# Kernel optimization log

Measured on AMD Instinct MI355X. Metric: run time of the kernel, lower is better.

Reference implementation:

```python
import jax, jax.numpy as jnp
import numpy as np

HW = 1048576   # h*w pixels (1024x1024)
C = 64         # feature channels
K = 4096       # number of superpixel clusters (min_superpixels)
H1 = 256       # KAN hidden width
NCLS = 16      # output classes
G = 5          # grid_size
SO = 3         # spline_order


def _grid(in_features):
    # torch: (arange(-SO, G+SO+1) * h + grid_range[0]).expand(in_features, -1)
    h = 2.0 / G  # (grid_range[1]-grid_range[0])/grid_size
    g = jnp.arange(-SO, G + SO + 1, dtype=jnp.float32) * h - 1.0  # [G+2*SO+1]
    return jnp.broadcast_to(g, (in_features, G + 2 * SO + 1))


def _b_splines(x, grid):
    # x: [N, in] -> bases: [N, in, G+SO]
    xg = x[:, :, None]
    bases = ((xg >= grid[:, :-1]) & (xg < grid[:, 1:])).astype(x.dtype)
    for k in range(1, SO + 1):
        left = (xg - grid[:, :-(k + 1)]) / (grid[:, k:-1] - grid[:, :-(k + 1)])
        right = (grid[:, k + 1:] - xg) / (grid[:, k + 1:] - grid[:, 1:-k])
        bases = left * bases[:, :, :-1] + right * bases[:, :, 1:]
    return bases


def _kan_layer(x, base_w, spline_w, spline_scaler):
    # KANLinear.forward: silu(x) @ base_w.T + bsplines(x) . (spline_w * scaler)
    grid = _grid(x.shape[-1])
    base_out = jax.nn.silu(x) @ base_w.T                      # [N, out]
    bases = _b_splines(x, grid)                               # [N, in, G+SO]
    scaled_w = spline_w * spline_scaler[:, :, None]           # [out, in, G+SO]
    spline_out = jnp.einsum('nig,oig->no', bases, scaled_w)
    return base_out + spline_out


def setup_inputs() -> dict:
    key = jax.random.key(0)
    ks = jax.random.split(key, 8)
    x = jax.random.normal(ks[0], (HW, C), dtype=jnp.float32)
    cls = jax.random.randint(ks[1], (HW,), 0, K, dtype=jnp.int32)
    bw1 = jax.random.normal(ks[2], (H1, C), dtype=jnp.float32) * 0.1
    sw1 = jax.random.normal(ks[3], (H1, C, G + SO), dtype=jnp.float32) * 0.1
    sc1 = jax.random.normal(ks[4], (H1, C), dtype=jnp.float32) * 0.1
    bw2 = jax.random.normal(ks[5], (NCLS, H1), dtype=jnp.float32) * 0.1
    sw2 = jax.random.normal(ks[6], (NCLS, H1, G + SO), dtype=jnp.float32) * 0.1
    sc2 = jax.random.normal(ks[7], (NCLS, H1), dtype=jnp.float32) * 0.1
    return dict(x=x, cls=cls, bw1=bw1, sw1=sw1, sc1=sc1, bw2=bw2, sw2=sw2, sc2=sc2)


def reference(x, cls, bw1, sw1, sc1, bw2, sw2, sc2):
    # VDSM scatter-mean aggregation: per-cluster mean of pixel features
    sums = jax.ops.segment_sum(x, cls, num_segments=K)                       # [K, C]
    cnt = jax.ops.segment_sum(jnp.ones((HW,), x.dtype), cls, num_segments=K)  # [K]
    clus_feat = sums / jnp.maximum(cnt, 1.0)[:, None]
    # WIC_Cls: stack of KANLinear layers on cluster features
    h = _kan_layer(clus_feat, bw1, sw1, sc1)
    out = _kan_layer(h, bw2, sw2, sc2)
    return out
```

## Files before the change

kernel.cpp:

```cpp
#include <hip/hip_runtime.h>

#define HW_N 1048576
#define C_IN 64
#define K_CLS 4096
#define H1_N 256
#define NCLS_N 16
#define SCAT_BLOCKS 256
#define ROWS_PER_SCAT (HW_N / SCAT_BLOCKS)
#define CAP 512
#define CLPB 16

__device__ __forceinline__ float silu_f(float x) {
  return x / (1.0f + expf(-x));
}

__device__ __forceinline__ void bspline8(float x, float* b) {
  float t[11];
#pragma unroll
  for (int j = 0; j < 11; ++j) {
    float g0 = 0.4f * (float)(j - 3) - 1.0f;
    float g1 = 0.4f * (float)(j - 2) - 1.0f;
    t[j] = (x >= g0 && x < g1) ? 1.0f : 0.0f;
  }
#pragma unroll
  for (int k = 1; k <= 3; ++k) {
#pragma unroll 10
    for (int j = 0; j + k < 11; ++j) {
      float gj   = 0.4f * (float)(j - 3) - 1.0f;
      float gj1  = 0.4f * (float)(j - 2) - 1.0f;
      float gjk  = 0.4f * (float)(j + k - 3) - 1.0f;
      float gjk1 = 0.4f * (float)(j + k - 2) - 1.0f;
      float left  = (x - gj) / (gjk - gj);
      float right = (gjk1 - x) / (gjk1 - gj1);
      t[j] = left * t[j] + right * t[j + 1];
    }
  }
#pragma unroll
  for (int g = 0; g < 8; ++g) b[g] = t[g];
}

__global__ __launch_bounds__(256) void transpose_w(
    const float* __restrict__ bw1, const float* __restrict__ sw1,
    const float* __restrict__ sc1, const float* __restrict__ bw2,
    const float* __restrict__ sw2, const float* __restrict__ sc2,
    float* __restrict__ bwt1, float* __restrict__ swt1,
    float* __restrict__ bwt2, float* __restrict__ swt2,
    int* __restrict__ ccnt) {
  int bid = blockIdx.x, tid = threadIdx.x;
  if (bid < C_IN) {
    int i = bid, o = tid;
    float sc = sc1[o * C_IN + i];
    bwt1[i * H1_N + o] = bw1[o * C_IN + i];
    const float4* src = (const float4*)&sw1[(size_t)(o * C_IN + i) * 8];
    float4 a = src[0], b = src[1];
    a.x *= sc; a.y *= sc; a.z *= sc; a.w *= sc;
    b.x *= sc; b.y *= sc; b.z *= sc; b.w *= sc;
    float4* dst = (float4*)&swt1[(size_t)(i * H1_N + o) * 8];
    dst[0] = a; dst[1] = b;
  } else if (bid < C_IN + H1_N / 2) {
    int gi = (bid - C_IN) * 2 + (tid >> 7);
    int t = tid & 127;
    int o = t >> 3, e = t & 7;
    swt2[(gi * NCLS_N + o) * 8 + e] =
        sw2[(size_t)(o * H1_N + gi) * 8 + e] * sc2[o * H1_N + gi];
    if (t < NCLS_N) bwt2[gi * NCLS_N + t] = bw2[t * H1_N + gi];
  } else {
    ccnt[(bid - C_IN - H1_N / 2) * 256 + tid] = 0;
  }
}

__global__ __launch_bounds__(1024) void scatter_atomic(
    const int* __restrict__ cls, int* __restrict__ ccnt,
    int* __restrict__ spk) {
  __shared__ int lhist[K_CLS];
  int b = blockIdx.x, tid = threadIdx.x;
  for (int c = tid; c < K_CLS; c += 1024) lhist[c] = 0;
  __syncthreads();
  int r0 = b * ROWS_PER_SCAT;
  for (int r = r0 + tid; r < r0 + ROWS_PER_SCAT; r += 1024)
    atomicAdd(&lhist[cls[r]], 1);
  __syncthreads();
  for (int c = tid; c < K_CLS; c += 1024) {
    int n = lhist[c];
    lhist[c] = n ? atomicAdd(&ccnt[c], n) : 0;
  }
  __syncthreads();
  for (int r = r0 + tid; r < r0 + ROWS_PER_SCAT; r += 1024) {
    int c = cls[r];
    int pos = atomicAdd(&lhist[c], 1);
    spk[(size_t)c * CAP + pos] = r;
  }
}

#define SM_BASES 0
#define SM_MEAN  33024
#define SM_SILU  (33024 + 4160)
#define SM_H     (33024 + 8320)
#define SM_SN    (33024 + 8320 + 16448)
#define SM_TOTAL (SM_SN + 64)

__global__ __launch_bounds__(256, 2) void mega(
    const float* __restrict__ x, const int* __restrict__ spk,
    const int* __restrict__ ccnt, const float* __restrict__ bwt1,
    const float* __restrict__ swt1, const float* __restrict__ bwt2,
    const float* __restrict__ swt2, float* __restrict__ out) {
  __shared__ __align__(16) char smem[SM_TOTAL];
  int* sidx = (int*)smem;
  float (*s_bases)[516] = (float(*)[516])smem;
  float (*mean_lds)[65] = (float(*)[65])(smem + SM_MEAN);
  float (*s_silu)[65]   = (float(*)[65])(smem + SM_SILU);
  float (*h_lds)[257]   = (float(*)[257])(smem + SM_H);
  int* sn = (int*)(smem + SM_SN);

  int bid = blockIdx.x, tid = threadIdx.x;

  {
    const int4* src = (const int4*)(spk + (size_t)bid * CLPB * CAP);
    int4* dst = (int4*)sidx;
#pragma unroll
    for (int k = 0; k < CLPB * CAP / 4 / 256; ++k)
      dst[tid + k * 256] = src[tid + k * 256];
    if (tid < CLPB) sn[tid] = ccnt[bid * CLPB + tid];
  }
  __syncthreads();

  {
    int cc = tid >> 4, q = tid & 15;
    int n = sn[cc];
    const int* sid = sidx + cc * CAP;
    const float4* x4 = (const float4*)x;
    float ax = 0.0f, ay = 0.0f, az = 0.0f, aw = 0.0f;
    int i = 0;
    for (; i + 7 < n; i += 8) {
      int p0 = sid[i],     p1 = sid[i + 1], p2 = sid[i + 2], p3 = sid[i + 3];
      int p4 = sid[i + 4], p5 = sid[i + 5], p6 = sid[i + 6], p7 = sid[i + 7];
      float4 v0 = x4[(size_t)p0 * 16 + q];
      float4 v1 = x4[(size_t)p1 * 16 + q];
      float4 v2 = x4[(size_t)p2 * 16 + q];
      float4 v3 = x4[(size_t)p3 * 16 + q];
      float4 v4 = x4[(size_t)p4 * 16 + q];
      float4 v5 = x4[(size_t)p5 * 16 + q];
      float4 v6 = x4[(size_t)p6 * 16 + q];
      float4 v7 = x4[(size_t)p7 * 16 + q];
      float tx0 = v0.x + v1.x, tx1 = v2.x + v3.x, tx2 = v4.x + v5.x, tx3 = v6.x + v7.x;
      float ty0 = v0.y + v1.y, ty1 = v2.y + v3.y, ty2 = v4.y + v5.y, ty3 = v6.y + v7.y;
      float tz0 = v0.z + v1.z, tz1 = v2.z + v3.z, tz2 = v4.z + v5.z, tz3 = v6.z + v7.z;
      float tw0 = v0.w + v1.w, tw1 = v2.w + v3.w, tw2 = v4.w + v5.w, tw3 = v6.w + v7.w;
      ax += (tx0 + tx1) + (tx2 + tx3);
      ay += (ty0 + ty1) + (ty2 + ty3);
      az += (tz0 + tz1) + (tz2 + tz3);
      aw += (tw0 + tw1) + (tw2 + tw3);
    }
    if (i < n) {
      int nm1 = n - 1;
      int i1 = i + 1, i2 = i + 2, i3 = i + 3, i4 = i + 4, i5 = i + 5,
          i6 = i + 6, i7 = i + 7;
      int p0 = sid[i];
      int p1 = sid[i1 < nm1 ? i1 : nm1];
      int p2 = sid[i2 < nm1 ? i2 : nm1];
      int p3 = sid[i3 < nm1 ? i3 : nm1];
      int p4 = sid[i4 < nm1 ? i4 : nm1];
      int p5 = sid[i5 < nm1 ? i5 : nm1];
      int p6 = sid[i6 < nm1 ? i6 : nm1];
      int p7 = sid[i7 < nm1 ? i7 : nm1];
      float4 v0 = x4[(size_t)p0 * 16 + q];
      float4 v1 = x4[(size_t)p1 * 16 + q];
      float4 v2 = x4[(size_t)p2 * 16 + q];
      float4 v3 = x4[(size_t)p3 * 16 + q];
      float4 v4 = x4[(size_t)p4 * 16 + q];
      float4 v5 = x4[(size_t)p5 * 16 + q];
      float4 v6 = x4[(size_t)p6 * 16 + q];
      float4 v7 = x4[(size_t)p7 * 16 + q];
      ax += v0.x; ay += v0.y; az += v0.z; aw += v0.w;
      if (i1 < n) { ax += v1.x; ay += v1.y; az += v1.z; aw += v1.w; }
      if (i2 < n) { ax += v2.x; ay += v2.y; az += v2.z; aw += v2.w; }
      if (i3 < n) { ax += v3.x; ay += v3.y; az += v3.z; aw += v3.w; }
      if (i4 < n) { ax += v4.x; ay += v4.y; az += v4.z; aw += v4.w; }
      if (i5 < n) { ax += v5.x; ay += v5.y; az += v5.z; aw += v5.w; }
      if (i6 < n) { ax += v6.x; ay += v6.y; az += v6.z; aw += v6.w; }
      if (i7 < n) { ax += v7.x; ay += v7.y; az += v7.z; aw += v7.w; }
    }
    float inv = 1.0f / fmaxf((float)n, 1.0f);
    mean_lds[cc][q * 4 + 0] = ax * inv;
    mean_lds[cc][q * 4 + 1] = ay * inv;
    mean_lds[cc][q * 4 + 2] = az * inv;
    mean_lds[cc][q * 4 + 3] = aw * inv;
  }
  __syncthreads();

  for (int p = tid; p < 16 * 64; p += 256) {
    int r = p >> 6, i = p & 63;
    float xv = mean_lds[r][i];
    s_silu[r][i] = silu_f(xv);
    float b[8];
    bspline8(xv, b);
    float4* dst = (float4*)&s_bases[r][i * 8];
    dst[0] = make_float4(b[0], b[1], b[2], b[3]);
    dst[1] = make_float4(b[4], b[5], b[6], b[7]);
  }
  __syncthreads();

  {
    int o = tid;
    float acc[16];
#pragma unroll
    for (int r = 0; r < 16; ++r) acc[r] = 0.0f;
    for (int i = 0; i < C_IN; ++i) {
      float wb = bwt1[i * H1_N + o];
      const float4* wp = (const float4*)&swt1[(size_t)(i * H1_N + o) * 8];
      float4 w0 = wp[0], w1 = wp[1];
#pragma unroll
      for (int r = 0; r < 16; ++r) {
        float sv = s_silu[r][i];
        const float4* bp = (const float4*)&s_bases[r][i * 8];
        float4 b0 = bp[0], b1 = bp[1];
        float a = acc[r];
        a = fmaf(sv, wb, a);
        a = fmaf(b0.x, w0.x, a); a = fmaf(b0.y, w0.y, a);
        a = fmaf(b0.z, w0.z, a); a = fmaf(b0.w, w0.w, a);
        a = fmaf(b1.x, w1.x, a); a = fmaf(b1.y, w1.y, a);
        a = fmaf(b1.z, w1.z, a); a = fmaf(b1.w, w1.w, a);
        acc[r] = a;
      }
    }
    __syncthreads();
#pragma unroll
    for (int r = 0; r < 16; ++r) h_lds[r][o] = acc[r];
  }
  __syncthreads();

  int o2 = tid & 15, rr = tid >> 4;
  float acc2 = 0.0f;
  for (int ic0 = 0; ic0 < H1_N; ic0 += 64) {
    for (int p = tid; p < 16 * 64; p += 256) {
      int r = p >> 6, i = p & 63;
      float xv = h_lds[r][ic0 + i];
      s_silu[r][i] = silu_f(xv);
      float b[8];
      bspline8(xv, b);
      float4* dst = (float4*)&s_bases[r][i * 8];
      dst[0] = make_float4(b[0], b[1], b[2], b[3]);
      dst[1] = make_float4(b[4], b[5], b[6], b[7]);
    }
    __syncthreads();

    for (int i = 0; i < 64; ++i) {
      int gi = ic0 + i;
      float wb = bwt2[gi * NCLS_N + o2];
      const float4* wp = (const float4*)&swt2[(gi * NCLS_N + o2) * 8];
      float4 w0 = wp[0], w1 = wp[1];
      float sv = s_silu[rr][i];
      const float4* bp = (const float4*)&s_bases[rr][i * 8];
      float4 b0 = bp[0], b1 = bp[1];
      float sp = b0.x * w0.x + b0.y * w0.y + b0.z * w0.z + b0.w * w0.w
               + b1.x * w1.x + b1.y * w1.y + b1.z * w1.z + b1.w * w1.w;
      acc2 = fmaf(sv, wb, acc2);
      acc2 += sp;
    }
    __syncthreads();
  }
  out[(bid * CLPB + rr) * NCLS_N + o2] = acc2;
}

extern "C" void kernel_launch(void* const* d_in, const int* in_sizes, int n_in,
                              void* d_out, int out_size, void* d_ws, size_t ws_size,
                              hipStream_t stream) {
  const float* x   = (const float*)d_in[0];
  const int*   cls = (const int*)d_in[1];
  const float* bw1 = (const float*)d_in[2];
  const float* sw1 = (const float*)d_in[3];
  const float* sc1 = (const float*)d_in[4];
  const float* bw2 = (const float*)d_in[5];
  const float* sw2 = (const float*)d_in[6];
  const float* sc2 = (const float*)d_in[7];
  float* out = (float*)d_out;

  int*   ccnt = (int*)d_ws;
  int*   spk  = ccnt + K_CLS;
  float* swt1 = (float*)(spk + K_CLS * CAP);
  float* bwt1 = swt1 + C_IN * H1_N * 8;
  float* swt2 = bwt1 + C_IN * H1_N;
  float* bwt2 = swt2 + H1_N * NCLS_N * 8;

  transpose_w<<<C_IN + H1_N / 2 + K_CLS / 256, 256, 0, stream>>>(
      bw1, sw1, sc1, bw2, sw2, sc2, bwt1, swt1, bwt2, swt2, ccnt);
  scatter_atomic<<<SCAT_BLOCKS, 1024, 0, stream>>>(cls, ccnt, spk);
  mega<<<K_CLS / CLPB, 256, 0, stream>>>(
      x, spk, ccnt, bwt1, swt1, bwt2, swt2, out);
}
```

Baseline: 157.8 us.

## Restructure mega kernel to 8 clusters per 512-thread block with split-K reductions

Halves clusters per block to 8 and doubles threads to 512, so each cluster gets a full wavefront. In the gather, four lane groups split the pixel indices and are combined with cross-lane shuffles, and the index list is read straight from global memory instead of being staged in LDS. Both KAN layers split their input dimension across thread halves or quarters and reduce the partial sums through shared memory. The aim is more parallelism and occupancy for the memory-bound gather, at the cost of more weight reloads per cluster and extra reduction steps.

New measurement: 128.3 us. 1.23x faster.

```diff
diff --git a/kernel.cpp b/kernel.cpp
--- a/kernel.cpp
+++ b/kernel.cpp
@@ -8,7 +8,7 @@
 #define SCAT_BLOCKS 256
 #define ROWS_PER_SCAT (HW_N / SCAT_BLOCKS)
 #define CAP 512
-#define CLPB 16
+#define CLPB 8
 
 __device__ __forceinline__ float silu_f(float x) {
   return x / (1.0f + expf(-x));
@@ -92,48 +92,33 @@
   }
 }
 
-#define SM_BASES 0
-#define SM_MEAN  33024
-#define SM_SILU  (33024 + 4160)
-#define SM_H     (33024 + 8320)
-#define SM_SN    (33024 + 8320 + 16448)
-#define SM_TOTAL (SM_SN + 64)
-
-__global__ __launch_bounds__(256, 2) void mega(
+__global__ __launch_bounds__(512, 4) void mega(
     const float* __restrict__ x, const int* __restrict__ spk,
     const int* __restrict__ ccnt, const float* __restrict__ bwt1,
     const float* __restrict__ swt1, const float* __restrict__ bwt2,
     const float* __restrict__ swt2, float* __restrict__ out) {
-  __shared__ __align__(16) char smem[SM_TOTAL];
-  int* sidx = (int*)smem;
-  float (*s_bases)[516] = (float(*)[516])smem;
-  float (*mean_lds)[65] = (float(*)[65])(smem + SM_MEAN);
-  float (*s_silu)[65]   = (float(*)[65])(smem + SM_SILU);
-  float (*h_lds)[257]   = (float(*)[257])(smem + SM_H);
-  int* sn = (int*)(smem + SM_SN);
+  __shared__ float s_bases[8][516];
+  __shared__ float s_silu[8][65];
+  __shared__ float mean_sacc[8][65];
+  __shared__ float h_lds[8][257];
+  __shared__ int sn[8];
 
   int bid = blockIdx.x, tid = threadIdx.x;
-
-  {
-    const int4* src = (const int4*)(spk + (size_t)bid * CLPB * CAP);
-    int4* dst = (int4*)sidx;
-#pragma unroll
-    for (int k = 0; k < CLPB * CAP / 4 / 256; ++k)
-      dst[tid + k * 256] = src[tid + k * 256];
-    if (tid < CLPB) sn[tid] = ccnt[bid * CLPB + tid];
-  }
-  __syncthreads();
-
-  {
-    int cc = tid >> 4, q = tid & 15;
-    int n = sn[cc];
-    const int* sid = sidx + cc * CAP;
+  int wv = tid >> 6, lane = tid & 63;
+  int g = lane >> 4, q = lane & 15;
+
+  if (tid < CLPB) sn[tid] = ccnt[bid * CLPB + tid];
+  __syncthreads();
+
+  {
+    int n = sn[wv];
+    const int* sid = spk + (size_t)(bid * CLPB + wv) * CAP;
     const float4* x4 = (const float4*)x;
     float ax = 0.0f, ay = 0.0f, az = 0.0f, aw = 0.0f;
-    int i = 0;
-    for (; i + 7 < n; i += 8) {
-      int p0 = sid[i],     p1 = sid[i + 1], p2 = sid[i + 2], p3 = sid[i + 3];
-      int p4 = sid[i + 4], p5 = sid[i + 5], p6 = sid[i + 6], p7 = sid[i + 7];
+    int i = g;
+    for (; i + 28 < n; i += 32) {
+      int p0 = sid[i],      p1 = sid[i + 4],  p2 = sid[i + 8],  p3 = sid[i + 12];
+      int p4 = sid[i + 16], p5 = sid[i + 20], p6 = sid[i + 24], p7 = sid[i + 28];
       float4 v0 = x4[(size_t)p0 * 16 + q];
       float4 v1 = x4[(size_t)p1 * 16 + q];
       float4 v2 = x4[(size_t)p2 * 16 + q];
@@ -153,8 +138,8 @@
     }
     if (i < n) {
       int nm1 = n - 1;
-      int i1 = i + 1, i2 = i + 2, i3 = i + 3, i4 = i + 4, i5 = i + 5,
-          i6 = i + 6, i7 = i + 7;
+      int i1 = i + 4, i2 = i + 8, i3 = i + 12, i4 = i + 16, i5 = i + 20,
+          i6 = i + 24, i7 = i + 28;
       int p0 = sid[i];
       int p1 = sid[i1 < nm1 ? i1 : nm1];
       int p2 = sid[i2 < nm1 ? i2 : nm1];
@@ -180,17 +165,23 @@
       if (i6 < n) { ax += v6.x; ay += v6.y; az += v6.z; aw += v6.w; }
       if (i7 < n) { ax += v7.x; ay += v7.y; az += v7.z; aw += v7.w; }
     }
-    float inv = 1.0f / fmaxf((float)n, 1.0f);
-    mean_lds[cc][q * 4 + 0] = ax * inv;
-    mean_lds[cc][q * 4 + 1] = ay * inv;
-    mean_lds[cc][q * 4 + 2] = az * inv;
-    mean_lds[cc][q * 4 + 3] = aw * inv;
-  }
-  __syncthreads();
-
-  for (int p = tid; p < 16 * 64; p += 256) {
-    int r = p >> 6, i = p & 63;
-    float xv = mean_lds[r][i];
+    ax += __shfl_xor(ax, 16); ax += __shfl_xor(ax, 32);
+    ay += __shfl_xor(ay, 16); ay += __shfl_xor(ay, 32);
+    az += __shfl_xor(az, 16); az += __shfl_xor(az, 32);
+    aw += __shfl_xor(aw, 16); aw += __shfl_xor(aw, 32);
+    if (g == 0) {
+      float inv = 1.0f / fmaxf((float)n, 1.0f);
+      mean_sacc[wv][q * 4 + 0] = ax * inv;
+      mean_sacc[wv][q * 4 + 1] = ay * inv;
+      mean_sacc[wv][q * 4 + 2] = az * inv;
+      mean_sacc[wv][q * 4 + 3] = aw * inv;
+    }
+  }
+  __syncthreads();
+
+  {
+    int r = tid >> 6, i = tid & 63;
+    float xv = mean_sacc[r][i];
     s_silu[r][i] = silu_f(xv);
     float b[8];
     bspline8(xv, b);
@@ -201,16 +192,17 @@
   __syncthreads();
 
   {
-    int o = tid;
-    float acc[16];
-#pragma unroll
-    for (int r = 0; r < 16; ++r) acc[r] = 0.0f;
-    for (int i = 0; i < C_IN; ++i) {
+    int o = tid & 255, ih = tid >> 8;
+    float acc[8];
+#pragma unroll
+    for (int r = 0; r < 8; ++r) acc[r] = 0.0f;
+    int i0 = ih * 32;
+    for (int i = i0; i < i0 + 32; ++i) {
       float wb = bwt1[i * H1_N + o];
       const float4* wp = (const float4*)&swt1[(size_t)(i * H1_N + o) * 8];
       float4 w0 = wp[0], w1 = wp[1];
 #pragma unroll
-      for (int r = 0; r < 16; ++r) {
+      for (int r = 0; r < 8; ++r) {
         float sv = s_silu[r][i];
         const float4* bp = (const float4*)&s_bases[r][i * 8];
         float4 b0 = bp[0], b1 = bp[1];
@@ -223,43 +215,57 @@
         acc[r] = a;
       }
     }
+    if (ih == 0) {
+#pragma unroll
+      for (int r = 0; r < 8; ++r) h_lds[r][o] = acc[r];
+    }
     __syncthreads();
-#pragma unroll
-    for (int r = 0; r < 16; ++r) h_lds[r][o] = acc[r];
-  }
-  __syncthreads();
-
-  int o2 = tid & 15, rr = tid >> 4;
-  float acc2 = 0.0f;
-  for (int ic0 = 0; ic0 < H1_N; ic0 += 64) {
-    for (int p = tid; p < 16 * 64; p += 256) {
-      int r = p >> 6, i = p & 63;
-      float xv = h_lds[r][ic0 + i];
-      s_silu[r][i] = silu_f(xv);
-      float b[8];
-      bspline8(xv, b);
-      float4* dst = (float4*)&s_bases[r][i * 8];
-      dst[0] = make_float4(b[0], b[1], b[2], b[3]);
-      dst[1] = make_float4(b[4], b[5], b[6], b[7]);
-    }
+    if (ih == 1) {
+#pragma unroll
+      for (int r = 0; r < 8; ++r) h_lds[r][o] += acc[r];
+    }
+  }
+  __syncthreads();
+
+  {
+    int o2 = tid & 15, rr = (tid >> 4) & 7, jh = tid >> 7;
+    float acc2 = 0.0f;
+    for (int ic0 = 0; ic0 < H1_N; ic0 += 64) {
+      {
+        int r = tid >> 6, i = tid & 63;
+        float xv = h_lds[r][ic0 + i];
+        s_silu[r][i] = silu_f(xv);
+        float b[8];
+        bspline8(xv, b);
+        float4* dst = (float4*)&s_bases[r][i * 8];
+        dst[0] = make_float4(b[0], b[1], b[2], b[3]);
+        dst[1] = make_float4(b[4], b[5], b[6], b[7]);
+      }
+      __syncthreads();
+      int ib = jh * 16;
+      for (int i = ib; i < ib + 16; ++i) {
+        int gi = ic0 + i;
+        float wb = bwt2[gi * NCLS_N + o2];
+        const float4* wp = (const float4*)&swt2[(gi * NCLS_N + o2) * 8];
+        float4 w0 = wp[0], w1 = wp[1];
+        float sv = s_silu[rr][i];
+        const float4* bp = (const float4*)&s_bases[rr][i * 8];
+        float4 b0 = bp[0], b1 = bp[1];
+        float sp = b0.x * w0.x + b0.y * w0.y + b0.z * w0.z + b0.w * w0.w
+                 + b1.x * w1.x + b1.y * w1.y + b1.z * w1.z + b1.w * w1.w;
+        acc2 = fmaf(sv, wb, acc2);
+        acc2 += sp;
+      }
+      __syncthreads();
+    }
+    float* sac = &mean_sacc[0][0];
+    sac[jh * 128 + rr * 16 + o2] = acc2;
     __syncthreads();
-
-    for (int i = 0; i < 64; ++i) {
-      int gi = ic0 + i;
-      float wb = bwt2[gi * NCLS_N + o2];
-      const float4* wp = (const float4*)&swt2[(gi * NCLS_N + o2) * 8];
-      float4 w0 = wp[0], w1 = wp[1];
-      float sv = s_silu[rr][i];
-      const float4* bp = (const float4*)&s_bases[rr][i * 8];
-      float4 b0 = bp[0], b1 = bp[1];
-      float sp = b0.x * w0.x + b0.y * w0.y + b0.z * w0.z + b0.w * w0.w
-               + b1.x * w1.x + b1.y * w1.y + b1.z * w1.z + b1.w * w1.w;
-      acc2 = fmaf(sv, wb, acc2);
-      acc2 += sp;
-    }
-    __syncthreads();
-  }
-  out[(bid * CLPB + rr) * NCLS_N + o2] = acc2;
+    if (tid < 128) {
+      float s = sac[tid] + sac[128 + tid] + sac[256 + tid] + sac[384 + tid];
+      out[(bid * CLPB + (tid >> 4)) * NCLS_N + (tid & 15)] = s;
+    }
+  }
 }
 
 extern "C" void kernel_launch(void* const* d_in, const int* in_sizes, int n_in,
@@ -285,6 +291,6 @@
   transpose_w<<<C_IN + H1_N / 2 + K_CLS / 256, 256, 0, stream>>>(
       bw1, sw1, sc1, bw2, sw2, sc2, bwt1, swt1, bwt2, swt2, ccnt);
   scatter_atomic<<<SCAT_BLOCKS, 1024, 0, stream>>>(cls, ccnt, spk);
-  mega<<<K_CLS / CLPB, 256, 0, stream>>>(
+  mega<<<K_CLS / CLPB, 512, 0, stream>>>(
       x, spk, ccnt, bwt1, swt1, bwt2, swt2, out);
 }
```
